# Performance work log

Hardware: AMD Instinct MI355X
Metric: run time of the kernel (lower is better)

## Reference

```python
import jax, jax.numpy as jnp
import numpy as np

ALPHA = 1.0
BETTA = 1.0
WEIGHT_ROTE = 0.5
WEIGHT_MSE = 0.5
EPS_MASK = 1e-8

B, D = 16384, 768


def setup_inputs() -> dict:
    key = jax.random.key(0)
    k1, k2, k3, k4 = jax.random.split(key, 4)
    return {
        "init_img_vec": jax.random.normal(k1, (B, 1, D), dtype=jnp.float32),
        "next_img_vec": jax.random.normal(k2, (B, 1, D), dtype=jnp.float32),
        "init_unclip": jax.random.normal(k3, (B, 1, D), dtype=jnp.float32),
        "pred_unclip": jax.random.normal(k4, (B, 1, D), dtype=jnp.float32),
    }


def _transform_loss(init_img_vec, next_img_vec, init_unclip, pred_unclip):
    diff_img = (init_img_vec - next_img_vec)[:, 0, :].astype(jnp.float32)      # [B, D]
    diff_unclip = init_unclip[:, 0, :].astype(jnp.float32) - pred_unclip[:, 0, :]

    # mask-compaction: rows with ||diff_img|| > 1e-8 are kept. We keep the full
    # batch (jit-safe) and weight the batch-mean by the mask; identical result.
    norm1 = jnp.linalg.norm(diff_img, axis=-1, keepdims=True)                  # [B, 1]
    mask = (norm1 > EPS_MASK)                                                  # [B, 1]
    mask_f = mask.astype(jnp.float32)
    cnt = jnp.maximum(jnp.sum(mask_f), 1.0)

    v1 = jnp.where(mask, diff_img, 1.0)   # safe values on masked-out rows
    v2 = diff_unclip

    # RotationVectors.angle / unit_vector
    n1 = v1 / jnp.linalg.norm(v1, axis=-1, keepdims=True)                      # [B, D]
    norm2 = jnp.linalg.norm(v2, axis=-1, keepdims=True)
    cos_ang = jnp.clip(jnp.sum(v1 * v2, axis=-1, keepdims=True)
                       / (jnp.linalg.norm(v1, axis=-1, keepdims=True) * norm2),
                       -1.0, 1.0)
    a = jnp.arccos(cos_ang)                                                    # [B, 1]

    w = v2 - n1 * jnp.sum(n1 * v2, axis=-1, keepdims=True)
    n2 = w / jnp.linalg.norm(w, axis=-1, keepdims=True)                        # [B, D]

    sin_a = jnp.sin(a)                 # [B, 1]
    cos_a_m1 = jnp.cos(a) - 1.0        # [B, 1]

    # transform = alpha*sin_a*(n2 n1^T - n1 n2^T) + betta*(cos_a-1)*(n1 n1^T + n2 n2^T)
    # u_transform = transform @ ones ; (M v^T) @ 1 = M * sum(v), so no DxD needed.
    s1 = jnp.sum(n1, axis=-1, keepdims=True)   # n1 . u
    s2 = jnp.sum(n2, axis=-1, keepdims=True)   # n2 . u
    u_transform = (ALPHA * sin_a * (n2 * s1 - n1 * s2)
                   + BETTA * cos_a_m1 * (n1 * s1 + n2 * s2))                   # [B, D]

    # loss_u: MSE(u_transform, 0), mean over masked rows -> [D]
    loss_u = jnp.sum((u_transform ** 2) * mask_f, axis=0) / cnt
    # loss_I: MSE(I @ ones, ones) = 0 exactly -> [D]
    loss_I = jnp.zeros((diff_img.shape[-1],), dtype=jnp.float32)

    loss_u = jnp.nan_to_num(loss_u, nan=0.0, posinf=0.1, neginf=-0.1)
    loss_I = jnp.nan_to_num(loss_I, nan=0.0, posinf=0.1, neginf=-0.1)

    # plain MSE over the FULL (unmasked) batch, mean over dim 0 -> [D]
    mse = jnp.mean((diff_img - diff_unclip) ** 2, axis=0) + loss_I

    return WEIGHT_ROTE * loss_u, WEIGHT_MSE * mse


def reference(init_img_vec, next_img_vec, init_unclip, pred_unclip):
    return _transform_loss(init_img_vec, next_img_vec, init_unclip, pred_unclip)
```

## Files before the change

kernel.cpp:

```cpp
#include <hip/hip_runtime.h>
#include <math.h>


constexpr int D      = 768;
constexpr int B_ROWS = 16384;
constexpr int BDIM   = 384;
constexpr int WPB    = BDIM / 64;
constexpr int NBLK   = 1024;
constexpr int RPB    = B_ROWS / NBLK;
constexpr int BDIM_R = 256;
constexpr int RG     = 64;
constexpr int NRG    = NBLK / RG;

constexpr size_t CNT_OFF = (size_t)NBLK * 2 * D;
constexpr size_t P2_OFF  = CNT_OFF + NBLK;

__global__ void zero_ws_kernel(float* __restrict__ ws, int n) {
    int i = blockIdx.x * blockDim.x + threadIdx.x;
    if (i < n) ws[i] = 0.0f;
}

template <bool PARTIALS>
__global__ __launch_bounds__(BDIM)
void transform_loss_main(const float* __restrict__ gA,
                         const float* __restrict__ gB,
                         const float* __restrict__ gC,
                         const float* __restrict__ gE,
                         float* __restrict__ ws)
{
    const int t    = threadIdx.x;
    const int lane = t & 63;
    const int wave = t >> 6;

    float au0 = 0.f, au1 = 0.f, am0 = 0.f, am1 = 0.f, lcnt = 0.f;

    __shared__ float red[2][WPB][8];

    size_t base = (size_t)blockIdx.x * RPB * D + (size_t)(2 * t);
    float2 va = *(const float2*)(gA + base);
    float2 vb = *(const float2*)(gB + base);
    float2 vc = *(const float2*)(gC + base);
    float2 ve = *(const float2*)(gE + base);

#pragma unroll
    for (int r = 0; r < RPB; ++r) {
        const float d1x = va.x - vb.x, d1y = va.y - vb.y;
        const float d2x = vc.x - ve.x, d2y = vc.y - ve.y;
        if (r + 1 < RPB) {
            base += D;
            va = *(const float2*)(gA + base);
            vb = *(const float2*)(gB + base);
            vc = *(const float2*)(gC + base);
            ve = *(const float2*)(gE + base);
        }
        float pA  = fmaf(d1x, d1x, d1y * d1y);
        float pC  = fmaf(d2x, d2x, d2y * d2y);
        float pAB = fmaf(d1x, d2x, d1y * d2y);
        float pS1 = d1x + d1y;
        float pS2 = d2x + d2y;
#pragma unroll
        for (int m = 1; m < 64; m <<= 1) {
            pA  += __shfl_xor(pA,  m);
            pC  += __shfl_xor(pC,  m);
            pAB += __shfl_xor(pAB, m);
            pS1 += __shfl_xor(pS1, m);
            pS2 += __shfl_xor(pS2, m);
        }
        if (lane == 0) {
            red[r & 1][wave][0] = pA;
            red[r & 1][wave][1] = pC;
            red[r & 1][wave][2] = pAB;
            red[r & 1][wave][3] = pS1;
            red[r & 1][wave][4] = pS2;
        }
        __syncthreads();
        float sA = 0.f, sC = 0.f, sAB = 0.f, sS1 = 0.f, sS2 = 0.f;
#pragma unroll
        for (int w = 0; w < WPB; ++w) {
            const float4 q = *(const float4*)&red[r & 1][w][0];
            sA  += q.x; sC += q.y; sAB += q.z; sS1 += q.w;
            sS2 += red[r & 1][w][4];
        }
        const float mdx = d1x - d2x, mdy = d1y - d2y;
        am0 = fmaf(mdx, mdx, am0);
        am1 = fmaf(mdy, mdy, am1);
        if (sA > 1e-16f) {
            lcnt += 1.f;
            const float nA  = sqrtf(sA);
            const float rA  = 1.f / nA;
            const float nC  = sqrtf(sC);
            float cosang = sAB / (nA * nC);
            cosang = fminf(fmaxf(cosang, -1.f), 1.f);
            const float sin_a = sqrtf(fmaxf(1.f - cosang * cosang, 0.f));
            const float cm1 = cosang - 1.f;
            const float k   = sAB / sA;
            const float W   = sC - sAB * k;
            const float rW  = 1.f / sqrtf(W);
            const float s1  = sS1 * rA;
            const float s2  = (sS2 - sS1 * k) * rW;
            const float p   = cm1 * s1 - sin_a * s2;
            const float q   = sin_a * s1 + cm1 * s2;
            const float c1  = p * rA - q * k * rW;
            const float c2  = q * rW;
            const float ux = fmaf(d1x, c1, d2x * c2);
            const float uy = fmaf(d1y, c1, d2y * c2);
            au0 = fmaf(ux, ux, au0);
            au1 = fmaf(uy, uy, au1);
        }
    }

    if (PARTIALS) {
        float* pb = ws + (size_t)blockIdx.x * (2 * D);
        *(float2*)(pb + 2 * t)     = make_float2(au0, au1);
        *(float2*)(pb + D + 2 * t) = make_float2(am0, am1);
        if (t == 0) ws[CNT_OFF + blockIdx.x] = lcnt;
    } else {
        atomicAdd(&ws[2 * t],         au0);
        atomicAdd(&ws[2 * t + 1],     au1);
        atomicAdd(&ws[D + 2 * t],     am0);
        atomicAdd(&ws[D + 2 * t + 1], am1);
        if (t == 0) atomicAdd(&ws[2 * D], lcnt);
    }
}

__global__ __launch_bounds__(BDIM_R)
void reduce_partials(const float* __restrict__ ws_in, float* __restrict__ ws_out)
{
    const int c  = blockIdx.x * BDIM_R + threadIdx.x;
    const int rg = blockIdx.y;
    if (c >= 2 * D) return;
    const float* p = ws_in + (size_t)rg * RG * (2 * D) + c;
    float s0 = 0.f, s1 = 0.f, s2 = 0.f, s3 = 0.f;
#pragma unroll 4
    for (int r = 0; r < RG; r += 4) {
        s0 += p[(size_t)(r + 0) * (2 * D)];
        s1 += p[(size_t)(r + 1) * (2 * D)];
        s2 += p[(size_t)(r + 2) * (2 * D)];
        s3 += p[(size_t)(r + 3) * (2 * D)];
    }
    ws_out[P2_OFF + (size_t)rg * (2 * D) + c] = (s0 + s1) + (s2 + s3);
}

__global__ __launch_bounds__(BDIM_R)
void finalize_tree(const float* __restrict__ ws, float* __restrict__ out)
{
    const int i = blockIdx.x * BDIM_R + threadIdx.x;
    float c = 0.f;
    for (int r = threadIdx.x; r < NBLK; r += BDIM_R) c += ws[CNT_OFF + r];
#pragma unroll
    for (int m = 1; m < 64; m <<= 1) c += __shfl_xor(c, m);
    __shared__ float sc[BDIM_R / 64];
    if ((threadIdx.x & 63) == 0) sc[threadIdx.x >> 6] = c;
    __syncthreads();
    float csum = 0.f;
#pragma unroll
    for (int wv = 0; wv < BDIM_R / 64; ++wv) csum += sc[wv];
    const float cnt = fmaxf(csum, 1.f);

    if (i >= 2 * D) return;
    float s = 0.f;
#pragma unroll
    for (int g = 0; g < NRG; ++g) s += ws[P2_OFF + (size_t)g * (2 * D) + i];

    if (i < D) {
        float lu = s / cnt;
        if (isnan(lu)) lu = 0.f;
        else if (isinf(lu)) lu = (lu > 0.f) ? 0.1f : -0.1f;
        out[i] = 0.5f * lu;
    } else {
        out[i] = 0.5f * (s * (1.f / 16384.f));
    }
}

__global__ __launch_bounds__(BDIM_R)
void finalize_atomic(const float* __restrict__ ws, float* __restrict__ out)
{
    const int i = blockIdx.x * BDIM_R + threadIdx.x;
    if (i >= 2 * D) return;
    const float cnt = fmaxf(ws[2 * D], 1.f);
    const float s = ws[i];
    if (i < D) {
        float lu = s / cnt;
        if (isnan(lu)) lu = 0.f;
        else if (isinf(lu)) lu = (lu > 0.f) ? 0.1f : -0.1f;
        out[i] = 0.5f * lu;
    } else {
        out[i] = 0.5f * (s * (1.f / 16384.f));
    }
}

extern "C" void kernel_launch(void* const* d_in, const int* in_sizes, int n_in,
                              void* d_out, int out_size, void* d_ws, size_t ws_size,
                              hipStream_t stream) {
    const float* init_img    = (const float*)d_in[0];
    const float* next_img    = (const float*)d_in[1];
    const float* init_unclip = (const float*)d_in[2];
    const float* pred_unclip = (const float*)d_in[3];
    float* ws  = (float*)d_ws;
    float* out = (float*)d_out;

    const size_t need = (P2_OFF + (size_t)NRG * 2 * D) * sizeof(float);
    if (ws_size >= need) {
        transform_loss_main<true><<<NBLK, BDIM, 0, stream>>>(
            init_img, next_img, init_unclip, pred_unclip, ws);
        reduce_partials<<<dim3((2 * D + BDIM_R - 1) / BDIM_R, NRG), BDIM_R, 0, stream>>>(ws, ws);
        finalize_tree<<<(2 * D + BDIM_R - 1) / BDIM_R, BDIM_R, 0, stream>>>(ws, out);
    } else {
        zero_ws_kernel<<<(2 * D + 1 + BDIM_R - 1) / BDIM_R, BDIM_R, 0, stream>>>(ws, 2 * D + 1);
        transform_loss_main<false><<<NBLK, BDIM, 0, stream>>>(
            init_img, next_img, init_unclip, pred_unclip, ws);
        finalize_atomic<<<(2 * D + BDIM_R - 1) / BDIM_R, BDIM_R, 0, stream>>>(ws, out);
    }
}
```

Measured before the change: 219.2 us.

## Map one row per wave via LDS double-buffered tiles to avoid block-wide row reductions

The main kernel now stages 4-row tiles of the differences into double-buffered LDS with float4 global loads, and each wave processes a whole 768-element row on its own. Row dot products and sums therefore need only a wave shuffle reduction, which removes the per-row block-wide __syncthreads and LDS reduction. Per-column accumulators are combined across waves through LDS at the end. The cost is more registers per thread (12 accumulators per kind plus prefetch buffers) and LDS traffic for staging.

```diff
diff --git a/kernel.cpp b/kernel.cpp
--- a/kernel.cpp
+++ b/kernel.cpp
@@ -4,10 +4,13 @@
 
 constexpr int D      = 768;
 constexpr int B_ROWS = 16384;
-constexpr int BDIM   = 384;
+constexpr int BDIM   = 256;
 constexpr int WPB    = BDIM / 64;
 constexpr int NBLK   = 1024;
 constexpr int RPB    = B_ROWS / NBLK;
+constexpr int TR     = 4;
+constexpr int NT     = RPB / TR;
+constexpr int CPL    = 3;
 constexpr int BDIM_R = 256;
 constexpr int RG     = 64;
 constexpr int NRG    = NBLK / RG;
@@ -21,7 +24,7 @@
 }
 
 template <bool PARTIALS>
-__global__ __launch_bounds__(BDIM)
+__global__ __launch_bounds__(BDIM, 3)
 void transform_loss_main(const float* __restrict__ gA,
                          const float* __restrict__ gB,
                          const float* __restrict__ gC,
@@ -32,32 +35,84 @@
     const int lane = t & 63;
     const int wave = t >> 6;
 
-    float au0 = 0.f, au1 = 0.f, am0 = 0.f, am1 = 0.f, lcnt = 0.f;
-
-    __shared__ float red[2][WPB][8];
-
-    size_t base = (size_t)blockIdx.x * RPB * D + (size_t)(2 * t);
-    float2 va = *(const float2*)(gA + base);
-    float2 vb = *(const float2*)(gB + base);
-    float2 vc = *(const float2*)(gC + base);
-    float2 ve = *(const float2*)(gE + base);
-
-#pragma unroll
-    for (int r = 0; r < RPB; ++r) {
-        const float d1x = va.x - vb.x, d1y = va.y - vb.y;
-        const float d2x = vc.x - ve.x, d2y = vc.y - ve.y;
-        if (r + 1 < RPB) {
-            base += D;
-            va = *(const float2*)(gA + base);
-            vb = *(const float2*)(gB + base);
-            vc = *(const float2*)(gC + base);
-            ve = *(const float2*)(gE + base);
-        }
-        float pA  = fmaf(d1x, d1x, d1y * d1y);
-        float pC  = fmaf(d2x, d2x, d2y * d2y);
-        float pAB = fmaf(d1x, d2x, d1y * d2y);
-        float pS1 = d1x + d1y;
-        float pS2 = d2x + d2y;
+    __shared__ float4 lds4[2][TR][2][192];
+    __shared__ float  cw[WPB];
+
+    float acc_u[CPL][4], acc_m[CPL][4];
+#pragma unroll
+    for (int k = 0; k < CPL; ++k)
+#pragma unroll
+        for (int j = 0; j < 4; ++j) { acc_u[k][j] = 0.f; acc_m[k][j] = 0.f; }
+    float lcnt = 0.f;
+
+    const size_t row0 = (size_t)blockIdx.x * RPB;
+
+    int srow[3], scc[3];
+#pragma unroll
+    for (int s = 0; s < 3; ++s) {
+        const int flat = s * BDIM + t;
+        srow[s] = flat / 192;
+        scc[s]  = flat % 192;
+    }
+
+    float4 la[3], lb[3], lc[3], le[3];
+
+#pragma unroll
+    for (int s = 0; s < 3; ++s) {
+        const size_t g = (row0 + srow[s]) * D + (size_t)(scc[s] * 4);
+        la[s] = *(const float4*)(gA + g);
+        lb[s] = *(const float4*)(gB + g);
+        lc[s] = *(const float4*)(gC + g);
+        le[s] = *(const float4*)(gE + g);
+    }
+#pragma unroll
+    for (int s = 0; s < 3; ++s) {
+        float4 d1, d2;
+        d1.x = la[s].x - lb[s].x; d1.y = la[s].y - lb[s].y;
+        d1.z = la[s].z - lb[s].z; d1.w = la[s].w - lb[s].w;
+        d2.x = lc[s].x - le[s].x; d2.y = lc[s].y - le[s].y;
+        d2.z = lc[s].z - le[s].z; d2.w = lc[s].w - le[s].w;
+        lds4[0][srow[s]][0][scc[s]] = d1;
+        lds4[0][srow[s]][1][scc[s]] = d2;
+    }
+
+    int cur = 0;
+    for (int tile = 0; tile < NT; ++tile) {
+        if (tile + 1 < NT) {
+#pragma unroll
+            for (int s = 0; s < 3; ++s) {
+                const size_t g = (row0 + (size_t)((tile + 1) * TR + srow[s])) * D
+                               + (size_t)(scc[s] * 4);
+                la[s] = *(const float4*)(gA + g);
+                lb[s] = *(const float4*)(gB + g);
+                lc[s] = *(const float4*)(gC + g);
+                le[s] = *(const float4*)(gE + g);
+            }
+        }
+        __syncthreads();
+
+        float4 v1[CPL], v2[CPL];
+#pragma unroll
+        for (int k = 0; k < CPL; ++k) {
+            v1[k] = lds4[cur][wave][0][k * 64 + lane];
+            v2[k] = lds4[cur][wave][1][k * 64 + lane];
+        }
+        float pA = 0.f, pC = 0.f, pAB = 0.f, pS1 = 0.f, pS2 = 0.f;
+#pragma unroll
+        for (int k = 0; k < CPL; ++k) {
+            const float x4[4] = {v1[k].x, v1[k].y, v1[k].z, v1[k].w};
+            const float y4[4] = {v2[k].x, v2[k].y, v2[k].z, v2[k].w};
+#pragma unroll
+            for (int j = 0; j < 4; ++j) {
+                pA  = fmaf(x4[j], x4[j], pA);
+                pC  = fmaf(y4[j], y4[j], pC);
+                pAB = fmaf(x4[j], y4[j], pAB);
+                pS1 += x4[j];
+                pS2 += y4[j];
+                const float md = x4[j] - y4[j];
+                acc_m[k][j] = fmaf(md, md, acc_m[k][j]);
+            }
+        }
 #pragma unroll
         for (int m = 1; m < 64; m <<= 1) {
             pA  += __shfl_xor(pA,  m);
@@ -66,60 +121,85 @@
             pS1 += __shfl_xor(pS1, m);
             pS2 += __shfl_xor(pS2, m);
         }
-        if (lane == 0) {
-            red[r & 1][wave][0] = pA;
-            red[r & 1][wave][1] = pC;
-            red[r & 1][wave][2] = pAB;
-            red[r & 1][wave][3] = pS1;
-            red[r & 1][wave][4] = pS2;
-        }
-        __syncthreads();
-        float sA = 0.f, sC = 0.f, sAB = 0.f, sS1 = 0.f, sS2 = 0.f;
-#pragma unroll
-        for (int w = 0; w < WPB; ++w) {
-            const float4 q = *(const float4*)&red[r & 1][w][0];
-            sA  += q.x; sC += q.y; sAB += q.z; sS1 += q.w;
-            sS2 += red[r & 1][w][4];
-        }
-        const float mdx = d1x - d2x, mdy = d1y - d2y;
-        am0 = fmaf(mdx, mdx, am0);
-        am1 = fmaf(mdy, mdy, am1);
-        if (sA > 1e-16f) {
+        if (pA > 1e-16f) {
             lcnt += 1.f;
-            const float nA  = sqrtf(sA);
+            const float nA  = sqrtf(pA);
             const float rA  = 1.f / nA;
-            const float nC  = sqrtf(sC);
-            float cosang = sAB / (nA * nC);
+            const float nC  = sqrtf(pC);
+            float cosang = pAB / (nA * nC);
             cosang = fminf(fmaxf(cosang, -1.f), 1.f);
             const float sin_a = sqrtf(fmaxf(1.f - cosang * cosang, 0.f));
             const float cm1 = cosang - 1.f;
-            const float k   = sAB / sA;
-            const float W   = sC - sAB * k;
+            const float kk  = pAB / pA;
+            const float W   = pC - pAB * kk;
             const float rW  = 1.f / sqrtf(W);
-            const float s1  = sS1 * rA;
-            const float s2  = (sS2 - sS1 * k) * rW;
+            const float s1  = pS1 * rA;
+            const float s2  = (pS2 - pS1 * kk) * rW;
             const float p   = cm1 * s1 - sin_a * s2;
             const float q   = sin_a * s1 + cm1 * s2;
-            const float c1  = p * rA - q * k * rW;
+            const float c1  = p * rA - q * kk * rW;
             const float c2  = q * rW;
-            const float ux = fmaf(d1x, c1, d2x * c2);
-            const float uy = fmaf(d1y, c1, d2y * c2);
-            au0 = fmaf(ux, ux, au0);
-            au1 = fmaf(uy, uy, au1);
-        }
-    }
-
+#pragma unroll
+            for (int k = 0; k < CPL; ++k) {
+                const float x4[4] = {v1[k].x, v1[k].y, v1[k].z, v1[k].w};
+                const float y4[4] = {v2[k].x, v2[k].y, v2[k].z, v2[k].w};
+#pragma unroll
+                for (int j = 0; j < 4; ++j) {
+                    const float u = fmaf(x4[j], c1, y4[j] * c2);
+                    acc_u[k][j] = fmaf(u, u, acc_u[k][j]);
+                }
+            }
+        }
+
+        if (tile + 1 < NT) {
+#pragma unroll
+            for (int s = 0; s < 3; ++s) {
+                float4 d1, d2;
+                d1.x = la[s].x - lb[s].x; d1.y = la[s].y - lb[s].y;
+                d1.z = la[s].z - lb[s].z; d1.w = la[s].w - lb[s].w;
+                d2.x = lc[s].x - le[s].x; d2.y = lc[s].y - le[s].y;
+                d2.z = lc[s].z - le[s].z; d2.w = lc[s].w - le[s].w;
+                lds4[cur ^ 1][srow[s]][0][scc[s]] = d1;
+                lds4[cur ^ 1][srow[s]][1][scc[s]] = d2;
+            }
+        }
+        cur ^= 1;
+    }
+
+    __syncthreads();
+    float4* f4 = (float4*)lds4;
+#pragma unroll
+    for (int k = 0; k < CPL; ++k) {
+        f4[wave * 192 + k * 64 + lane] =
+            make_float4(acc_u[k][0], acc_u[k][1], acc_u[k][2], acc_u[k][3]);
+        f4[768 + wave * 192 + k * 64 + lane] =
+            make_float4(acc_m[k][0], acc_m[k][1], acc_m[k][2], acc_m[k][3]);
+    }
+    if (lane == 0) cw[wave] = lcnt;
+    __syncthreads();
+
+    const float* f = (const float*)f4;
     if (PARTIALS) {
         float* pb = ws + (size_t)blockIdx.x * (2 * D);
-        *(float2*)(pb + 2 * t)     = make_float2(au0, au1);
-        *(float2*)(pb + D + 2 * t) = make_float2(am0, am1);
-        if (t == 0) ws[CNT_OFF + blockIdx.x] = lcnt;
-    } else {
-        atomicAdd(&ws[2 * t],         au0);
-        atomicAdd(&ws[2 * t + 1],     au1);
-        atomicAdd(&ws[D + 2 * t],     am0);
-        atomicAdd(&ws[D + 2 * t + 1], am1);
-        if (t == 0) atomicAdd(&ws[2 * D], lcnt);
+#pragma unroll
+        for (int i = 0; i < 3; ++i) {
+            const int c = t + i * 256;
+            const float su = (f[c] + f[768 + c]) + (f[1536 + c] + f[2304 + c]);
+            const float sm = (f[3072 + c] + f[3840 + c]) + (f[4608 + c] + f[5376 + c]);
+            pb[c]     = su;
+            pb[D + c] = sm;
+        }
+        if (t == 0) ws[CNT_OFF + blockIdx.x] = (cw[0] + cw[1]) + (cw[2] + cw[3]);
+    } else {
+#pragma unroll
+        for (int i = 0; i < 3; ++i) {
+            const int c = t + i * 256;
+            const float su = (f[c] + f[768 + c]) + (f[1536 + c] + f[2304 + c]);
+            const float sm = (f[3072 + c] + f[3840 + c]) + (f[4608 + c] + f[5376 + c]);
+            atomicAdd(&ws[c], su);
+            atomicAdd(&ws[D + c], sm);
+        }
+        if (t == 0) atomicAdd(&ws[2 * D], (cw[0] + cw[1]) + (cw[2] + cw[3]));
     }
 }
 
```

Measured after the change: 210.9 us. -3.8%, faster.
